# Optimization experiments

Hardware: AMD Instinct MI355X
Metric: run time of the kernel (lower is better)

The kernel has to match this reference:

```python
import jax, jax.numpy as jnp
import numpy as np

ALPHA = 1.0
EPS = 1e-6

NUM_CLASSES = 100000
FEAT_DIM = 256
BATCH = 8192


def setup_inputs() -> dict:
    key = jax.random.key(0)
    k1, k2 = jax.random.split(key)
    features = jax.random.normal(k1, (BATCH, FEAT_DIM), dtype=jnp.float32)
    target = jax.random.randint(k2, (BATCH,), 0, NUM_CLASSES, dtype=jnp.int64)
    # centers bank initialized to zeros as in the torch module
    centers = jnp.zeros((NUM_CLASSES, FEAT_DIM), dtype=jnp.float32)
    return {"features": features, "target": target, "centers": centers}


def reference(features, target, centers):
    # gather per-sample class centers: [B, D]
    centers_batch = centers[target]
    # MSE loss over all elements (nn.MSELoss default reduction='mean')
    diff = centers_batch - features  # [B, D]
    center_loss = jnp.mean(diff * diff)
    # per-class appearance counts, gathered back per sample
    counts = jax.ops.segment_sum(
        jnp.ones((target.shape[0],), dtype=jnp.float32), target,
        num_segments=NUM_CLASSES)  # [C]
    appear = counts[target]  # [B]
    # per-sample scaled update, scatter-added into the centers bank
    upd = ALPHA * diff / (appear + EPS)[:, None]  # [B, D]
    delta = jax.ops.segment_sum(upd, target, num_segments=NUM_CLASSES)  # [C, D]
    new_centers = centers - delta
    return center_loss, new_centers
```

## Files before the change

### kernel.cpp

```cpp
#include <hip/hip_runtime.h>

#define BATCH   8192
#define FEAT    256
#define NCLASS  100000
#define EPS_C   1e-6f

#define NC_ELEMS (NCLASS * FEAT)
#define NVEC (NC_ELEMS / 4)
#define COPY_BLOCKS (NVEC / 256)

__global__ void copy_build_kernel(const float* __restrict__ centers,
                                  float* __restrict__ out ,
                                  const int* __restrict__ target,
                                  int* __restrict__ head,
                                  int* __restrict__ next) {
    int v = blockIdx.x * blockDim.x + threadIdx.x;
    const float4* cvec = (const float4*)centers;
    float4 cv = cvec[v];
    int lane = threadIdx.x & 63;
    float prev = __shfl_up(cv.w, 1);
    if (lane == 0) {
        prev = (v > 0) ? centers[4 * v - 1] : 0.0f;
    }
    float4 ov;
    ov.x = prev; ov.y = cv.x; ov.z = cv.y; ov.w = cv.z;
    ((float4*)out)[v] = ov;
    if (v == 0) out[NC_ELEMS] = centers[NC_ELEMS - 1];

    if (blockIdx.x < (BATCH / 256)) {
        int b = blockIdx.x * 256 + threadIdx.x;
        int t = target[b];
        next[b] = atomicExch(&head[t], b);
    }
}

__global__ void scatter_kernel(const float* __restrict__ features,
                               const int* __restrict__ target,
                               const float* __restrict__ centers,
                               const int* __restrict__ head,
                               const int* __restrict__ next,
                               float* __restrict__ partials,
                               float* __restrict__ out ) {
    int b = blockIdx.x;
    int d = threadIdx.x;
    int t = target[b];
    float c = centers[t * FEAT + d];
    float f = features[b * FEAT + d];
    float diff = c - f;

    float sq = diff * diff;
    #pragma unroll
    for (int off = 32; off > 0; off >>= 1) sq += __shfl_down(sq, off, 64);
    __shared__ float red[4];
    int wave = threadIdx.x >> 6;
    int lane = threadIdx.x & 63;
    if (lane == 0) red[wave] = sq;
    __syncthreads();
    if (threadIdx.x == 0) {
        partials[b] = red[0] + red[1] + red[2] + red[3];
    }

    if (head[t] == b) {
        float sumf = f;
        int n = 1;
        for (int s = next[b]; s != -1; s = next[s]) {
            sumf += features[s * FEAT + d];
            n++;
        }
        float nf = (float)n;
        out[1 + t * FEAT + d] = c - (nf * c - sumf) / (nf + EPS_C);
    }
}

__global__ void finalize_kernel(const float* __restrict__ partials,
                                float* __restrict__ out0) {
    float s = 0.0f;
    for (int i = threadIdx.x; i < BATCH; i += 256) s += partials[i];
    #pragma unroll
    for (int off = 32; off > 0; off >>= 1) s += __shfl_down(s, off, 64);
    __shared__ float red[4];
    int wave = threadIdx.x >> 6;
    int lane = threadIdx.x & 63;
    if (lane == 0) red[wave] = s;
    __syncthreads();
    if (threadIdx.x == 0) {
        out0[0] = (red[0] + red[1] + red[2] + red[3]) / (float)(BATCH * FEAT);
    }
}

extern "C" void kernel_launch(void* const* d_in, const int* in_sizes, int n_in,
                              void* d_out, int out_size, void* d_ws, size_t ws_size,
                              hipStream_t stream) {
    const float* features = (const float*)d_in[0];
    const int*   target   = (const int*)d_in[1];
    const float* centers  = (const float*)d_in[2];
    float* out = (float*)d_out;

    int*   head     = (int*)d_ws;
    int*   next     = head + NCLASS;
    float* partials = (float*)(next + BATCH);

    hipMemsetAsync(head, 0xFF, NCLASS * sizeof(int), stream);
    copy_build_kernel<<<COPY_BLOCKS, 256, 0, stream>>>(centers, out, target, head, next);
    scatter_kernel<<<BATCH, FEAT, 0, stream>>>(features, target, centers,
                                               head, next, partials, out);
    finalize_kernel<<<1, 256, 0, stream>>>(partials, out);
}
```

Baseline: 206.7 us.

## Fuse center copy and per-class update into one class-major kernel

Moves linked-list construction into its own small kernel. A single fused kernel then walks every class row, applies the per-class update to the row when it has samples, computes each sample's squared-error partial, and writes the shifted output through LDS. This removes the separate scatter pass over the batch and the second write of updated rows on top of the full copy. The cost is that every block also reads head[] and must recompute the last element of the previous block's row for the one-element output offset.

```diff
diff --git a/kernel.cpp b/kernel.cpp
--- a/kernel.cpp
+++ b/kernel.cpp
@@ -7,69 +7,84 @@
 
 #define NC_ELEMS (NCLASS * FEAT)
 #define NVEC (NC_ELEMS / 4)
-#define COPY_BLOCKS (NVEC / 256)
+#define FUSED_BLOCKS (NVEC / 256)
 
-__global__ void copy_build_kernel(const float* __restrict__ centers,
-                                  float* __restrict__ out ,
-                                  const int* __restrict__ target,
-                                  int* __restrict__ head,
-                                  int* __restrict__ next) {
-    int v = blockIdx.x * blockDim.x + threadIdx.x;
-    const float4* cvec = (const float4*)centers;
-    float4 cv = cvec[v];
-    int lane = threadIdx.x & 63;
-    float prev = __shfl_up(cv.w, 1);
-    if (lane == 0) {
-        prev = (v > 0) ? centers[4 * v - 1] : 0.0f;
-    }
-    float4 ov;
-    ov.x = prev; ov.y = cv.x; ov.z = cv.y; ov.w = cv.z;
-    ((float4*)out)[v] = ov;
-    if (v == 0) out[NC_ELEMS] = centers[NC_ELEMS - 1];
-
-    if (blockIdx.x < (BATCH / 256)) {
-        int b = blockIdx.x * 256 + threadIdx.x;
-        int t = target[b];
-        next[b] = atomicExch(&head[t], b);
-    }
+__global__ void build_kernel(const int* __restrict__ target,
+                             int* __restrict__ head,
+                             int* __restrict__ next) {
+    int b = blockIdx.x * blockDim.x + threadIdx.x;
+    if (b < BATCH) next[b] = atomicExch(&head[target[b]], b);
 }
 
-__global__ void scatter_kernel(const float* __restrict__ features,
-                               const int* __restrict__ target,
-                               const float* __restrict__ centers,
-                               const int* __restrict__ head,
-                               const int* __restrict__ next,
-                               float* __restrict__ partials,
-                               float* __restrict__ out ) {
-    int b = blockIdx.x;
-    int d = threadIdx.x;
-    int t = target[b];
-    float c = centers[t * FEAT + d];
-    float f = features[b * FEAT + d];
-    float diff = c - f;
+__global__ void fused_kernel(const float* __restrict__ centers,
+                             const float* __restrict__ features,
+                             const int* __restrict__ head,
+                             const int* __restrict__ next,
+                             float* __restrict__ partials,
+                             float* __restrict__ out ) {
+    __shared__ float lds[1025];
+    int w = threadIdx.x >> 6;
+    int l = threadIdx.x & 63;
+    int r = blockIdx.x * 4 + w;
 
-    float sq = diff * diff;
-    #pragma unroll
-    for (int off = 32; off > 0; off >>= 1) sq += __shfl_down(sq, off, 64);
-    __shared__ float red[4];
-    int wave = threadIdx.x >> 6;
-    int lane = threadIdx.x & 63;
-    if (lane == 0) red[wave] = sq;
-    __syncthreads();
-    if (threadIdx.x == 0) {
-        partials[b] = red[0] + red[1] + red[2] + red[3];
-    }
-
-    if (head[t] == b) {
-        float sumf = f;
-        int n = 1;
-        for (int s = next[b]; s != -1; s = next[s]) {
-            sumf += features[s * FEAT + d];
+    float4 c4 = ((const float4*)(centers + (size_t)r * FEAT))[l];
+    float4 n4 = c4;
+    int h = head[r];
+    if (h != -1) {
+        float4 sumf = {0.f, 0.f, 0.f, 0.f};
+        int n = 0;
+        for (int s = h; s != -1; s = next[s]) {
+            float4 f4 = ((const float4*)(features + (size_t)s * FEAT))[l];
+            sumf.x += f4.x; sumf.y += f4.y; sumf.z += f4.z; sumf.w += f4.w;
+            float dx = c4.x - f4.x, dy = c4.y - f4.y;
+            float dz = c4.z - f4.z, dw = c4.w - f4.w;
+            float sq = dx*dx + dy*dy + dz*dz + dw*dw;
+            #pragma unroll
+            for (int off = 32; off > 0; off >>= 1) sq += __shfl_down(sq, off, 64);
+            if (l == 0) partials[s] = sq;
             n++;
         }
         float nf = (float)n;
-        out[1 + t * FEAT + d] = c - (nf * c - sumf) / (nf + EPS_C);
+        float inv = 1.0f / (nf + EPS_C);
+        n4.x = c4.x - (nf * c4.x - sumf.x) * inv;
+        n4.y = c4.y - (nf * c4.y - sumf.y) * inv;
+        n4.z = c4.z - (nf * c4.z - sumf.z) * inv;
+        n4.w = c4.w - (nf * c4.w - sumf.w) * inv;
     }
+
+    int base = 1 + w * 256 + 4 * l;
+    lds[base + 0] = n4.x; lds[base + 1] = n4.y;
+    lds[base + 2] = n4.z; lds[base + 3] = n4.w;
+
+    if (threadIdx.x == 0) {
+        float val = 0.0f;
+        if (blockIdx.x > 0) {
+            int rp = blockIdx.x * 4 - 1;
+            float c = centers[(size_t)rp * FEAT + 255];
+            val = c;
+            int hp = head[rp];
+            if (hp != -1) {
+                float sf = 0.0f; int n = 0;
+                for (int s = hp; s != -1; s = next[s]) {
+                    sf += features[(size_t)s * FEAT + 255]; n++;
+                }
+                float nf = (float)n;
+                val = c - (nf * c - sf) / (nf + EPS_C);
+            }
+        }
+        lds[0] = val;
+    }
+    if (blockIdx.x == FUSED_BLOCKS - 1 && threadIdx.x == 255) {
+        out[NC_ELEMS] = n4.w;
+    }
+
+    __syncthreads();
+
+    int t = threadIdx.x;
+    float4 ov;
+    ov.x = lds[4*t + 0]; ov.y = lds[4*t + 1];
+    ov.z = lds[4*t + 2]; ov.w = lds[4*t + 3];
+    ((float4*)out)[(size_t)blockIdx.x * 256 + t] = ov;
 }
 
 __global__ void finalize_kernel(const float* __restrict__ partials,
@@ -101,8 +116,8 @@
     float* partials = (float*)(next + BATCH);
 
     hipMemsetAsync(head, 0xFF, NCLASS * sizeof(int), stream);
-    copy_build_kernel<<<COPY_BLOCKS, 256, 0, stream>>>(centers, out, target, head, next);
-    scatter_kernel<<<BATCH, FEAT, 0, stream>>>(features, target, centers,
-                                               head, next, partials, out);
+    build_kernel<<<(BATCH + 255) / 256, 256, 0, stream>>>(target, head, next);
+    fused_kernel<<<FUSED_BLOCKS, 256, 0, stream>>>(centers, features, head, next,
+                                                   partials, out);
     finalize_kernel<<<1, 256, 0, stream>>>(partials, out);
 }
```

New measurement: 196.4 us. 1.05x faster.
